# Kernel tuning notes

Measured on AMD Instinct MI355X. Metric: run time of the kernel, lower is better.

The kernel has to match this reference:

```python
import jax, jax.numpy as jnp
import numpy as np

DIM = 384
HEADS = 12
HEAD_DIM = DIM // HEADS
WS = 7


def setup_inputs() -> dict:
    key = jax.random.key(0)
    k0, k1, k2, k3, k4 = jax.random.split(key, 5)
    x = jax.random.normal(k0, (16, DIM, 56, 56), dtype=jnp.float32)
    s = 1.0 / np.sqrt(DIM)
    Wqkv = jax.random.normal(k1, (DIM, 3 * DIM), dtype=jnp.float32) * s
    bqkv = jax.random.normal(k2, (3 * DIM,), dtype=jnp.float32) * 0.01
    Wproj = jax.random.normal(k3, (DIM, DIM), dtype=jnp.float32) * s
    bproj = jax.random.normal(k4, (DIM,), dtype=jnp.float32) * 0.01
    return {"x": x, "Wqkv": Wqkv, "bqkv": bqkv, "Wproj": Wproj, "bproj": bproj}


def _window_attention(x, Wqkv, bqkv, Wproj, bproj):
    B, D, H, W = x.shape
    x = jnp.transpose(x, (0, 2, 3, 1))  # (B, H, W, D)
    pad_h = (WS - H % WS) % WS
    pad_w = (WS - W % WS) % WS
    if pad_h or pad_w:
        x = jnp.pad(x, ((0, 0), (0, pad_h), (0, pad_w), (0, 0)))
    Hp, Wp = x.shape[1], x.shape[2]
    nH, nW = Hp // WS, Wp // WS
    # window partition: (B*nH*nW, WS*WS, D)
    xw = x.reshape(B, nH, WS, nW, WS, D).transpose(0, 1, 3, 2, 4, 5)
    windows = xw.reshape(B * nH * nW, WS * WS, D)
    BnW, N, _ = windows.shape
    qkv = windows @ Wqkv + bqkv  # (BnW, N, 3D)
    qkv = qkv.reshape(BnW, N, 3, HEADS, HEAD_DIM).transpose(2, 0, 3, 1, 4)
    q, k, v = qkv[0], qkv[1], qkv[2]  # (BnW, heads, N, hd)
    scale = HEAD_DIM ** -0.5
    attn = jnp.einsum('bhnd,bhmd->bhnm', q, k) * scale
    attn = jax.nn.softmax(attn, axis=-1)
    out = jnp.einsum('bhnm,bhmd->bhnd', attn, v)  # (BnW, heads, N, hd)
    out = out.transpose(0, 2, 1, 3).reshape(BnW, N, D)
    out = out @ Wproj + bproj
    # window reverse
    x = out.reshape(B, nH, nW, WS, WS, D).transpose(0, 1, 3, 2, 4, 5)
    x = x.reshape(B, Hp, Wp, D)
    if pad_h or pad_w:
        x = x[:, :H, :W, :]
    return jnp.transpose(x, (0, 3, 1, 2))  # (B, D, H, W)


def reference(x, Wqkv, bqkv, Wproj, bproj):
    return _window_attention(x, Wqkv, bqkv, Wproj, bproj)
```

## Files before the change

### kernel.cpp

```cpp
#include <hip/hip_runtime.h>

#define TOK     50176
#define NQKV    1152
#define DMODEL  384
#define HW      3136
#define NWIN    1024

typedef __bf16 bf16x8 __attribute__((ext_vector_type(8)));
typedef float  f32x4  __attribute__((ext_vector_type(4)));

__device__ __forceinline__ __bf16 f2bf(float f) {
  unsigned u = __float_as_uint(f);
  u += 0x7fffu + ((u >> 16) & 1u);
  unsigned short s = (unsigned short)(u >> 16);
  return __builtin_bit_cast(__bf16, s);
}
__device__ __forceinline__ unsigned short f2bfu(float f) {
  return __builtin_bit_cast(unsigned short, f2bf(f));
}
__device__ __forceinline__ float bf2f(__bf16 b) {
  return __uint_as_float(((unsigned)__builtin_bit_cast(unsigned short, b)) << 16);
}
__device__ __forceinline__ void gload_lds16(const void* g, void* l) {
  __builtin_amdgcn_global_load_lds(
      (const __attribute__((address_space(1))) unsigned int*)g,
      (__attribute__((address_space(3))) unsigned int*)l, 16, 0, 0);
}

__global__ __launch_bounds__(256) void gather_x(const float* __restrict__ x,
                                                __bf16* __restrict__ Xw) {
  __shared__ __bf16 lt[392 * 48];
  const int ct = blockIdx.x, hr = blockIdx.y, b = blockIdx.z;
  const int tid = threadIdx.x;
  const float* xb = x + ((size_t)(b * 384 + ct * 48)) * HW + hr * 7 * 56;

  for (int u = tid; u < 48 * 7 * 14; u += 256) {
    const int ch = u / 98, rem = u % 98;
    const int h7 = rem / 14, w4 = rem % 14;
    const float4 v = *(const float4*)&xb[(size_t)ch * HW + h7 * 56 + 4 * w4];
    const float vv[4] = {v.x, v.y, v.z, v.w};
#pragma unroll
    for (int e = 0; e < 4; ++e) {
      const int w = 4 * w4 + e;
      const int t = (w / 7) * 49 + h7 * 7 + (w % 7);
      lt[t * 48 + ch] = f2bf(vv[e]);
    }
  }
  __syncthreads();

  const size_t tokbase = (size_t)(b * 64 + hr * 8) * 49;
  for (int u = tid; u < 392 * 6; u += 256) {
    const int t = u / 6, c6 = u % 6;
    const bf16x8 vv = *(const bf16x8*)&lt[t * 48 + 8 * c6];
    *(bf16x8*)&Xw[(tokbase + t) * DMODEL + ct * 48 + 8 * c6] = vv;
  }
}

__global__ __launch_bounds__(256) void unscatter(const __bf16* __restrict__ P,
                                                 float* __restrict__ out) {
  __shared__ __bf16 lt[392 * 48];
  const int ct = blockIdx.x, hr = blockIdx.y, b = blockIdx.z;
  const int tid = threadIdx.x;
  const size_t tokbase = (size_t)(b * 64 + hr * 8) * 49;

  for (int u = tid; u < 392 * 6; u += 256) {
    const int t = u / 6, c6 = u % 6;
    *(bf16x8*)&lt[t * 48 + 8 * c6] =
        *(const bf16x8*)&P[(tokbase + t) * DMODEL + ct * 48 + 8 * c6];
  }
  __syncthreads();

  float* ob = out + ((size_t)(b * 384 + ct * 48)) * HW + hr * 7 * 56;
  for (int u = tid; u < 48 * 98; u += 256) {
    const int ch = u / 98, rem = u % 98;
    const int h7 = rem / 14, w4 = rem % 14;
    float4 o;
    float* oo = (float*)&o;
#pragma unroll
    for (int e = 0; e < 4; ++e) {
      const int w = 4 * w4 + e;
      const int t = (w / 7) * 49 + h7 * 7 + (w % 7);
      oo[e] = bf2f(lt[t * 48 + ch]);
    }
    *(float4*)&ob[(size_t)ch * HW + h7 * 56 + 4 * w4] = o;
  }
}

__global__ void conv_w(const float* __restrict__ Wqkv, const float* __restrict__ Wproj,
                       __bf16* __restrict__ WqkvT, __bf16* __restrict__ WprojT) {
  const int idx = blockIdx.x * 256 + threadIdx.x;
  if (idx < DMODEL * NQKV) {
    const int k = idx / NQKV, n = idx % NQKV;
    WqkvT[(size_t)n * DMODEL + k] = f2bf(Wqkv[idx]);
  }
  if (idx < DMODEL * DMODEL) {
    const int k = idx / DMODEL, n = idx % DMODEL;
    WprojT[(size_t)n * DMODEL + k] = f2bf(Wproj[idx]);
  }
}

__global__ __launch_bounds__(256, 2) void gemm256(const __bf16* __restrict__ A,
                                                  const __bf16* __restrict__ BT,
                                                  const float* __restrict__ bias,
                                                  __bf16* __restrict__ Cout, int Ncols) {
  __shared__ __align__(16) __bf16 As[2][256 * 32];
  __shared__ __align__(16) __bf16 Bs[2][128 * 32];
  const int tid  = threadIdx.x;
  const int lane = tid & 63;
  const int wid  = tid >> 6;

  const int nwg  = gridDim.x * gridDim.y;
  const int orig = blockIdx.y * gridDim.x + blockIdx.x;
  const int q    = nwg >> 3, r = nwg & 7;
  const int xcd  = orig & 7, pos = orig >> 3;
  const int start = (xcd < r) ? xcd * (q + 1) : r * (q + 1) + (xcd - r) * q;
  const int w    = start + pos;
  const int bn   = (w % gridDim.x) << 7;
  const int bm   = (w / gridDim.x) << 8;

  const __bf16* a0 = A  + (size_t)(bm +       (tid >> 2)) * DMODEL + ((tid & 3) << 3);
  const __bf16* a1 = A  + (size_t)(bm +  64 + (tid >> 2)) * DMODEL + ((tid & 3) << 3);
  const __bf16* a2 = A  + (size_t)(bm + 128 + (tid >> 2)) * DMODEL + ((tid & 3) << 3);
  const __bf16* a3 = A  + (size_t)(bm + 192 + (tid >> 2)) * DMODEL + ((tid & 3) << 3);
  const __bf16* b0 = BT + (size_t)(bn +       (tid >> 2)) * DMODEL + ((tid & 3) << 3);
  const __bf16* b1 = BT + (size_t)(bn +  64 + (tid >> 2)) * DMODEL + ((tid & 3) << 3);

  const int wm = (wid >> 1) << 7;
  const int wn = (wid & 1) << 6;
  const int lrow = lane & 15;
  const int lk8  = (lane >> 4) << 3;

  f32x4 acc[4][8] = {};

  auto stage = [&](int buf, int kt) {
    const int koff = kt << 5;
    gload_lds16(a0 + koff, &As[buf][(wid << 9)]);
    gload_lds16(a1 + koff, &As[buf][2048 + (wid << 9)]);
    gload_lds16(a2 + koff, &As[buf][4096 + (wid << 9)]);
    gload_lds16(a3 + koff, &As[buf][6144 + (wid << 9)]);
    gload_lds16(b0 + koff, &Bs[buf][(wid << 9)]);
    gload_lds16(b1 + koff, &Bs[buf][2048 + (wid << 9)]);
  };

  stage(0, 0);
#pragma unroll 1
  for (int kt = 0; kt < 12; ++kt) {
    __syncthreads();
    if (kt + 1 < 12) stage((kt + 1) & 1, kt + 1);
    const __bf16* pA = &As[kt & 1][(wm + lrow) * 32 + lk8];
    const __bf16* pB = &Bs[kt & 1][(wn + lrow) * 32 + lk8];
    bf16x8 av[8], bv[4];
#pragma unroll
    for (int i = 0; i < 8; ++i) av[i] = *(const bf16x8*)(pA + i * 16 * 32);
#pragma unroll
    for (int j = 0; j < 4; ++j) bv[j] = *(const bf16x8*)(pB + j * 16 * 32);
#pragma unroll
    for (int i = 0; i < 8; ++i)
#pragma unroll
      for (int j = 0; j < 4; ++j)
        acc[j][i] = __builtin_amdgcn_mfma_f32_16x16x32_bf16(bv[j], av[i], acc[j][i], 0, 0, 0);
  }

  const int lr = lane & 15, g = lane >> 4;
  const int tok0 = bm + wm + lr;
  const int ch0  = bn + wn + (g << 2);

#pragma unroll
  for (int j = 0; j < 4; ++j) {
    const int ch = ch0 + 16 * j;
    const float4 b4 = *(const float4*)&bias[ch];
#pragma unroll
    for (int i = 0; i < 8; ++i) {
      const int token = tok0 + 16 * i;
      ushort4 pk;
      pk.x = f2bfu(acc[j][i][0] + b4.x);
      pk.y = f2bfu(acc[j][i][1] + b4.y);
      pk.z = f2bfu(acc[j][i][2] + b4.z);
      pk.w = f2bfu(acc[j][i][3] + b4.w);
      *(ushort4*)&Cout[(size_t)token * Ncols + ch] = pk;
    }
  }
}

__global__ __launch_bounds__(64) void attn_mfma(const __bf16* __restrict__ qkv,
                                                __bf16* __restrict__ attnO) {
  __shared__ __align__(16) __bf16 lds[96 * 72];
  __bf16* p_lds = lds;
  __bf16* vt    = lds + 64 * 72;

  const int lane = threadIdx.x;
  const int win  = blockIdx.x;
  const int h    = blockIdx.y;
  const int lr = lane & 15, g = lane >> 4;
  const size_t rowbase = (size_t)win * 49;

  int rr[4];
#pragma unroll
  for (int f = 0; f < 4; ++f) rr[f] = (16 * f + lr > 48) ? 48 : (16 * f + lr);

  const int co = h * 32 + 8 * g;

  bf16x8 av[4], bv[4];
#pragma unroll
  for (int f = 0; f < 4; ++f) {
    const __bf16* rp = qkv + (rowbase + rr[f]) * NQKV + co;
    av[f] = *(const bf16x8*)(rp + 384);
    bv[f] = *(const bf16x8*)(rp);
  }

  ushort4 vreg[7];
#pragma unroll
  for (int u = 0; u < 7; ++u) {
    const int unit = lane + (u << 6);
    if (unit < 392) {
      const int k = unit >> 3, dq = unit & 7;
      vreg[u] = *(const ushort4*)(qkv + (rowbase + k) * NQKV + 768 + h * 32 + 4 * dq);
    }
  }

  f32x4 acc[4][4] = {};
#pragma unroll
  for (int i = 0; i < 4; ++i)
#pragma unroll
    for (int j = 0; j < 4; ++j)
      acc[i][j] = __builtin_amdgcn_mfma_f32_16x16x32_bf16(av[i], bv[j], acc[i][j], 0, 0, 0);

  const float scale = 0.17677669529663687f;
#pragma unroll
  for (int i = 0; i < 4; ++i)
#pragma unroll
    for (int j = 0; j < 4; ++j)
#pragma unroll
      for (int r = 0; r < 4; ++r) {
        float v = acc[i][j][r] * scale;
        if (i == 3 && (4 * g + r) != 0) v = -1e30f;
        acc[i][j][r] = v;
      }

#pragma unroll
  for (int u = 0; u < 7; ++u) {
    const int unit = lane + (u << 6);
    if (unit < 392) {
      const int k = unit >> 3, dq = unit & 7;
      const ushort4 vv = vreg[u];
      vt[(4 * dq + 0) * 72 + k] = __builtin_bit_cast(__bf16, vv.x);
      vt[(4 * dq + 1) * 72 + k] = __builtin_bit_cast(__bf16, vv.y);
      vt[(4 * dq + 2) * 72 + k] = __builtin_bit_cast(__bf16, vv.z);
      vt[(4 * dq + 3) * 72 + k] = __builtin_bit_cast(__bf16, vv.w);
    }
  }

#pragma unroll
  for (int j = 0; j < 4; ++j) {
    float mx = -1e30f;
#pragma unroll
    for (int i = 0; i < 4; ++i)
#pragma unroll
      for (int r = 0; r < 4; ++r) mx = fmaxf(mx, acc[i][j][r]);
    mx = fmaxf(mx, __shfl_xor(mx, 16));
    mx = fmaxf(mx, __shfl_xor(mx, 32));
    float sum = 0.f;
#pragma unroll
    for (int i = 0; i < 4; ++i)
#pragma unroll
      for (int r = 0; r < 4; ++r) {
        const float e = __expf(acc[i][j][r] - mx);
        acc[i][j][r] = e;
        sum += e;
      }
    sum += __shfl_xor(sum, 16);
    sum += __shfl_xor(sum, 32);
    const float inv = 1.f / sum;
#pragma unroll
    for (int i = 0; i < 4; ++i) {
      ushort4 pk;
      pk.x = f2bfu(acc[i][j][0] * inv);
      pk.y = f2bfu(acc[i][j][1] * inv);
      pk.z = f2bfu(acc[i][j][2] * inv);
      pk.w = f2bfu(acc[i][j][3] * inv);
      *(ushort4*)&p_lds[(16 * j + lr) * 72 + 16 * i + 4 * g] = pk;
    }
  }

  f32x4 o[2][4] = {};
#pragma unroll
  for (int ks = 0; ks < 2; ++ks) {
    bf16x8 a2[2], b2[4];
#pragma unroll
    for (int i2 = 0; i2 < 2; ++i2)
      a2[i2] = *(const bf16x8*)&vt[(16 * i2 + lr) * 72 + 32 * ks + 8 * g];
#pragma unroll
    for (int j2 = 0; j2 < 4; ++j2)
      b2[j2] = *(const bf16x8*)&p_lds[(16 * j2 + lr) * 72 + 32 * ks + 8 * g];
#pragma unroll
    for (int i2 = 0; i2 < 2; ++i2)
#pragma unroll
      for (int j2 = 0; j2 < 4; ++j2)
        o[i2][j2] = __builtin_amdgcn_mfma_f32_16x16x32_bf16(a2[i2], b2[j2], o[i2][j2], 0, 0, 0);
  }

#pragma unroll
  for (int j2 = 0; j2 < 4; ++j2) {
    const int q = 16 * j2 + lr;
    if (q <= 48) {
#pragma unroll
      for (int i2 = 0; i2 < 2; ++i2) {
        ushort4 ok;
        ok.x = f2bfu(o[i2][j2][0]);
        ok.y = f2bfu(o[i2][j2][1]);
        ok.z = f2bfu(o[i2][j2][2]);
        ok.w = f2bfu(o[i2][j2][3]);
        *(ushort4*)&attnO[(rowbase + q) * DMODEL + h * 32 + 16 * i2 + 4 * g] = ok;
      }
    }
  }
}

extern "C" void kernel_launch(void* const* d_in, const int* in_sizes, int n_in,
                              void* d_out, int out_size, void* d_ws, size_t ws_size,
                              hipStream_t stream) {
  const float* x     = (const float*)d_in[0];
  const float* Wqkv  = (const float*)d_in[1];
  const float* bqkv  = (const float*)d_in[2];
  const float* Wproj = (const float*)d_in[3];
  const float* bproj = (const float*)d_in[4];
  float* out = (float*)d_out;

  char* ws = (char*)d_ws;
  __bf16* Xw     = (__bf16*)ws;  ws += (size_t)TOK * DMODEL * 2;
  __bf16* qkvb   = (__bf16*)ws;  ws += (size_t)TOK * NQKV * 2;
  __bf16* attnO  = (__bf16*)ws;  ws += (size_t)TOK * DMODEL * 2;
  __bf16* attnP  = (__bf16*)ws;  ws += (size_t)TOK * DMODEL * 2;
  __bf16* WqkvT  = (__bf16*)ws;  ws += (size_t)NQKV * DMODEL * 2;
  __bf16* WprojT = (__bf16*)ws;

  gather_x<<<dim3(8, 8, 16), 256, 0, stream>>>(x, Xw);
  conv_w<<<1728, 256, 0, stream>>>(Wqkv, Wproj, WqkvT, WprojT);
  gemm256<<<dim3(NQKV / 128, TOK / 256), 256, 0, stream>>>(Xw, WqkvT, bqkv, qkvb, NQKV);
  attn_mfma<<<dim3(NWIN, 12), 64, 0, stream>>>(qkvb, attnO);
  gemm256<<<dim3(DMODEL / 128, TOK / 256), 256, 0, stream>>>(attnO, WprojT, bproj, attnP, DMODEL);
  unscatter<<<dim3(8, 8, 16), 256, 0, stream>>>(attnP, out);
}
```

Measured before the change: 225.0 us.

## Stage GEMM epilogue through LDS for coalesced stores and raise MFMA priority

The GEMM epilogue now writes bias-added bf16 results into a per-wave LDS tile, then reads them back as 16-byte rows. This turns the old scattered 8-byte stores into row-contiguous global writes. The shared buffers are merged into one array so the epilogue can reuse that space, and s_setprio is raised around the MFMA block. The launch_bounds occupancy hint is also dropped. The padded LDS row stride of 70 elements means the 16-byte LDS accesses are not naturally aligned, and the extra LDS round trip and syncs add latency.

```diff
diff --git a/kernel.cpp b/kernel.cpp
--- a/kernel.cpp
+++ b/kernel.cpp
@@ -99,12 +99,11 @@
   }
 }
 
-__global__ __launch_bounds__(256, 2) void gemm256(const __bf16* __restrict__ A,
-                                                  const __bf16* __restrict__ BT,
-                                                  const float* __restrict__ bias,
-                                                  __bf16* __restrict__ Cout, int Ncols) {
-  __shared__ __align__(16) __bf16 As[2][256 * 32];
-  __shared__ __align__(16) __bf16 Bs[2][128 * 32];
+__global__ __launch_bounds__(256) void gemm256(const __bf16* __restrict__ A,
+                                               const __bf16* __restrict__ BT,
+                                               const float* __restrict__ bias,
+                                               __bf16* __restrict__ Cout, int Ncols) {
+  __shared__ __align__(16) __bf16 sm[2 * (256 * 32 + 128 * 32)];
   const int tid  = threadIdx.x;
   const int lane = tid & 63;
   const int wid  = tid >> 6;
@@ -134,12 +133,14 @@
 
   auto stage = [&](int buf, int kt) {
     const int koff = kt << 5;
-    gload_lds16(a0 + koff, &As[buf][(wid << 9)]);
-    gload_lds16(a1 + koff, &As[buf][2048 + (wid << 9)]);
-    gload_lds16(a2 + koff, &As[buf][4096 + (wid << 9)]);
-    gload_lds16(a3 + koff, &As[buf][6144 + (wid << 9)]);
-    gload_lds16(b0 + koff, &Bs[buf][(wid << 9)]);
-    gload_lds16(b1 + koff, &Bs[buf][2048 + (wid << 9)]);
+    __bf16* As = sm + buf * (384 * 32);
+    __bf16* Bs = As + 256 * 32;
+    gload_lds16(a0 + koff, As + (wid << 9));
+    gload_lds16(a1 + koff, As + 2048 + (wid << 9));
+    gload_lds16(a2 + koff, As + 4096 + (wid << 9));
+    gload_lds16(a3 + koff, As + 6144 + (wid << 9));
+    gload_lds16(b0 + koff, Bs + (wid << 9));
+    gload_lds16(b1 + koff, Bs + 2048 + (wid << 9));
   };
 
   stage(0, 0);
@@ -147,38 +148,58 @@
   for (int kt = 0; kt < 12; ++kt) {
     __syncthreads();
     if (kt + 1 < 12) stage((kt + 1) & 1, kt + 1);
-    const __bf16* pA = &As[kt & 1][(wm + lrow) * 32 + lk8];
-    const __bf16* pB = &Bs[kt & 1][(wn + lrow) * 32 + lk8];
+    const __bf16* As = sm + (kt & 1) * (384 * 32);
+    const __bf16* Bs = As + 256 * 32;
+    const __bf16* pA = As + (wm + lrow) * 32 + lk8;
+    const __bf16* pB = Bs + (wn + lrow) * 32 + lk8;
     bf16x8 av[8], bv[4];
 #pragma unroll
     for (int i = 0; i < 8; ++i) av[i] = *(const bf16x8*)(pA + i * 16 * 32);
 #pragma unroll
     for (int j = 0; j < 4; ++j) bv[j] = *(const bf16x8*)(pB + j * 16 * 32);
+    __builtin_amdgcn_s_setprio(1);
 #pragma unroll
     for (int i = 0; i < 8; ++i)
 #pragma unroll
       for (int j = 0; j < 4; ++j)
         acc[j][i] = __builtin_amdgcn_mfma_f32_16x16x32_bf16(bv[j], av[i], acc[j][i], 0, 0, 0);
-  }
-
+    __builtin_amdgcn_s_setprio(0);
+  }
+
+  __syncthreads();
   const int lr = lane & 15, g = lane >> 4;
-  const int tok0 = bm + wm + lr;
-  const int ch0  = bn + wn + (g << 2);
-
-#pragma unroll
-  for (int j = 0; j < 4; ++j) {
-    const int ch = ch0 + 16 * j;
-    const float4 b4 = *(const float4*)&bias[ch];
-#pragma unroll
-    for (int i = 0; i < 8; ++i) {
-      const int token = tok0 + 16 * i;
-      ushort4 pk;
-      pk.x = f2bfu(acc[j][i][0] + b4.x);
-      pk.y = f2bfu(acc[j][i][1] + b4.y);
-      pk.z = f2bfu(acc[j][i][2] + b4.z);
-      pk.w = f2bfu(acc[j][i][3] + b4.w);
-      *(ushort4*)&Cout[(size_t)token * Ncols + ch] = pk;
-    }
+  __bf16* epi = sm + wid * (64 * 70);
+
+  float4 b4[4];
+#pragma unroll
+  for (int j = 0; j < 4; ++j)
+    b4[j] = *(const float4*)&bias[bn + wn + (g << 2) + 16 * j];
+
+  const int rrow = lane >> 3;
+  const int rcol = (lane & 7) << 3;
+
+#pragma unroll
+  for (int half = 0; half < 2; ++half) {
+#pragma unroll
+    for (int j = 0; j < 4; ++j)
+#pragma unroll
+      for (int i = 0; i < 4; ++i) {
+        const int ii = (half << 2) + i;
+        ushort4 pk;
+        pk.x = f2bfu(acc[j][ii][0] + b4[j].x);
+        pk.y = f2bfu(acc[j][ii][1] + b4[j].y);
+        pk.z = f2bfu(acc[j][ii][2] + b4[j].z);
+        pk.w = f2bfu(acc[j][ii][3] + b4[j].w);
+        *(ushort4*)&epi[(lr + (i << 4)) * 70 + (g << 2) + (j << 4)] = pk;
+      }
+    asm volatile("s_waitcnt lgkmcnt(0)" ::: "memory");
+#pragma unroll
+    for (int p = 0; p < 8; ++p) {
+      const int trow = (p << 3) + rrow;
+      const bf16x8 v = *(const bf16x8*)&epi[trow * 70 + rcol];
+      *(bf16x8*)&Cout[(size_t)(bm + wm + (half << 6) + trow) * Ncols + bn + wn + rcol] = v;
+    }
+    asm volatile("s_waitcnt lgkmcnt(0)" ::: "memory");
   }
 }
 
```

Result: slower. 262.7 us (+16.7%).
